# Optimization experiments

Hardware: AMD Instinct MI355X
Metric: run time of the kernel (lower is better)

The kernel has to match this reference:

```python
import math
import jax, jax.numpy as jnp
import numpy as np

B, L, DM = 2, 1024, 1024
STATE, EXPAND, CONV, DTR = 16, 2, 4, 8
INNER = DM * EXPAND          # 2048
NFFT = L // 2 + 1            # 513


def _silu(v):
    return v * jax.nn.sigmoid(v)


def setup_inputs() -> dict:
    key = jax.random.key(0)
    ks = jax.random.split(key, 12)
    s = lambda k, shape, sc=0.02: (jax.random.normal(k, shape, jnp.float32) * sc)
    # dt_proj bias initialized like the torch module: exp(U(0,1)*(log dt_max - log dt_min) + log dt_min)
    inv_dt = jnp.exp(jax.random.uniform(ks[10], (INNER,), jnp.float32)
                     * (math.log(0.1) - math.log(0.001)) + math.log(0.001))
    return {
        "x": jax.random.normal(ks[0], (B, L, DM), jnp.float32),
        "in_proj_w": s(ks[1], (2 * INNER, DM)),
        "conv_w": s(ks[2], (INNER, 1, CONV), 0.1),      # depthwise conv kernel
        "conv_b": jnp.zeros((INNER,), jnp.float32),
        "A_log": jnp.tile(jnp.log(jnp.arange(1, STATE + 1, dtype=jnp.float32)), (INNER, 1)),
        "D": jnp.ones((INNER,), jnp.float32),
        "x_proj_w": s(ks[3], (DTR + 2 * STATE, INNER)),
        "dt_proj_w": s(ks[4], (INNER, DTR)),
        "dt_proj_b": inv_dt,
        "filter_real": s(ks[5], (INNER, NFFT)),
        "filter_imag": s(ks[6], (INNER, NFFT)),
        "spectral_decay": jnp.ones((INNER,), jnp.float32) * 0.01,
        "fusion_w": s(ks[7], (INNER, 2 * INNER)),
        "fusion_b": jnp.zeros((INNER,), jnp.float32),
        "out_proj_w": s(ks[8], (DM, INNER)),
        "ln_gamma": jnp.ones((DM,), jnp.float32),
        "ln_beta": jnp.zeros((DM,), jnp.float32),
    }


def reference(x, in_proj_w, conv_w, conv_b, A_log, D, x_proj_w, dt_proj_w, dt_proj_b,
              filter_real, filter_imag, spectral_decay, fusion_w, fusion_b,
              out_proj_w, ln_gamma, ln_beta):
    residual = x
    xz = x @ in_proj_w.T                                   # [B,L,2*INNER]
    x_inner, z = xz[..., :INNER], xz[..., INNER:]
    z = _silu(z)

    # ---- SSM path ----
    xc = jnp.swapaxes(x_inner, 1, 2)                       # [B,E,L]
    xc = jax.lax.conv_general_dilated(
        xc, conv_w, (1,), [(CONV - 1, 0)],                 # causal depthwise conv (pad-left == torch pad + truncate)
        dimension_numbers=("NCH", "OIH", "NCH"),
        feature_group_count=INNER) + conv_b[None, :, None]
    x_conv = jnp.swapaxes(_silu(xc), 1, 2)                 # [B,L,E]

    x_dbc = x_conv @ x_proj_w.T                            # [B,L,DTR+2S]
    dt_x = x_dbc[..., :DTR]
    Bm = x_dbc[..., DTR:DTR + STATE]                       # [B,L,S]
    Cm = x_dbc[..., DTR + STATE:]                          # [B,L,S]
    dt = jax.nn.softplus(dt_x @ dt_proj_w.T + dt_proj_b)   # [B,L,E]
    A = -jnp.exp(A_log)                                    # [E,S]
    dA = jnp.exp(dt[..., None] * A)                        # [B,L,E,S]
    dBx = (dt * x_conv)[..., None] * Bm[:, :, None, :]     # [B,L,E,S]

    def step(h, inp):
        dA_t, dBx_t, C_t = inp
        h = dA_t * h + dBx_t                               # [B,E,S]
        return h, jnp.einsum('bes,bs->be', h, C_t)

    h0 = jnp.zeros((B, INNER, STATE), x.dtype)
    _, ys = jax.lax.scan(step, h0,
                         (jnp.swapaxes(dA, 0, 1), jnp.swapaxes(dBx, 0, 1), jnp.swapaxes(Cm, 0, 1)))
    y_ssm = jnp.swapaxes(ys, 0, 1) + x_conv * D            # [B,L,E]

    # ---- Spectral path ----
    xf = jnp.fft.rfft(jnp.swapaxes(x_inner, 1, 2), axis=-1)        # [B,E,NFFT]
    freqs = jnp.linspace(0.0, 1.0, NFFT)
    filt = (filter_real + 1j * filter_imag) * jnp.exp(-spectral_decay[:, None] * freqs[None, :])
    y_spec = jnp.swapaxes(jnp.fft.irfft(xf * filt[None], n=L, axis=-1), 1, 2)  # [B,L,E]

    # ---- Gated fusion ----
    g = jax.nn.sigmoid(jnp.concatenate([y_ssm, y_spec], -1) @ fusion_w.T + fusion_b)
    y = g * y_ssm + (1.0 - g) * y_spec
    y = y * z
    out = y @ out_proj_w.T + residual                      # [B,L,DM]

    mu = out.mean(-1, keepdims=True)
    var = out.var(-1, keepdims=True)
    return (out - mu) / jnp.sqrt(var + 1e-5) * ln_gamma + ln_beta
```

## Files before the change

### kernel.cpp

```cpp
#include <hip/hip_runtime.h>
#include <math.h>

#define B_ 2
#define L_ 1024
#define DM_ 1024
#define STATE_ 16
#define CONV_ 4
#define DTR_ 8
#define INNER_ 2048
#define M_ (B_*L_)
#define MD_ (B_*INNER_)
#define NFFT_ 513
#define NFP_ 1152
#define NCH_ 32
#define CHL_ 32
#define SK_ 32
#define KSL_ (2048/SK_)

typedef unsigned short u16;
typedef __attribute__((ext_vector_type(8))) short short8;
typedef __attribute__((ext_vector_type(8))) __bf16 bf16x8;
typedef __attribute__((ext_vector_type(4))) float f32x4;

__device__ __forceinline__ float frcp_(float x) { return __builtin_amdgcn_rcpf(x); }
__device__ __forceinline__ float fexp_(float x) { return __expf(x); }
__device__ __forceinline__ float fsigm_(float x) { return frcp_(1.f + __expf(-x)); }
__device__ __forceinline__ float fsilu_(float x) { return x * frcp_(1.f + __expf(-x)); }
__device__ __forceinline__ float fsoftplus_(float v) {
  return (v > 20.f) ? v : __logf(1.f + __expf(v));
}
__device__ __forceinline__ u16 f2bf(float f) {
  union { float f; unsigned u; } v; v.f = f;
  unsigned r = v.u + 0x7fffu + ((v.u >> 16) & 1u);
  return (u16)(r >> 16);
}
__device__ __forceinline__ float bf2f(u16 h) {
  union { unsigned u; float f; } v; v.u = ((unsigned)h) << 16;
  return v.f;
}
__device__ __forceinline__ void gload16(const void* g, void* l) {
  __builtin_amdgcn_global_load_lds(
      (const __attribute__((address_space(1))) unsigned*)g,
      (__attribute__((address_space(3))) unsigned*)l, 16, 0, 0);
}
__device__ __forceinline__ f32x4 mfma_bf16(short8 a, short8 b, f32x4 c) {
  return __builtin_amdgcn_mfma_f32_16x16x32_bf16(
      __builtin_bit_cast(bf16x8, a), __builtin_bit_cast(bf16x8, b), c, 0, 0, 0);
}

#define CVT_N0 2097152
#define CVT_N1 6291456
#define CVT_N2 14680064
#define CVT_NT 16777216
__global__ __launch_bounds__(256) void cvt4_k(
    const float* __restrict__ s0, const float* __restrict__ s1,
    const float* __restrict__ s2, const float* __restrict__ s3,
    u16* __restrict__ out)
{
  int i = (blockIdx.x*256 + threadIdx.x) * 4;
  const float* src; int off;
  if (i < CVT_N0)      { src = s0; off = 0; }
  else if (i < CVT_N1) { src = s1; off = CVT_N0; }
  else if (i < CVT_N2) { src = s2; off = CVT_N1; }
  else                 { src = s3; off = CVT_N2; }
  float4 v = *(const float4*)(src + (i - off));
  ushort4 o;
  o.x = f2bf(v.x); o.y = f2bf(v.y); o.z = f2bf(v.z); o.w = f2bf(v.w);
  *(ushort4*)(out + i) = o;
}

template<int TM, int TN, int EPI>
__global__ __launch_bounds__((TM/64)*(TN/32)*64) void mgemm_k(
    const u16* __restrict__ Ab, const u16* __restrict__ Bb,
    void* __restrict__ Cout, int K, int ldc,
    const float* __restrict__ aux0, const u16* __restrict__ aux1,
    const float* __restrict__ aux2, const float* __restrict__ aux3)
{
  constexpr int WN   = TN/32;
  constexpr int NW   = (TM/64)*WN;
  constexpr int NTHR = NW*64;
  __shared__ __align__(16) u16 As[2][TM*64];
  __shared__ __align__(16) u16 Bs[2][TN*64];
  const int t = threadIdx.x;
  const int lane = t & 63;
  const int w = t >> 6;
  const int wm = w / WN, wn = w % WN;
  const int M0 = blockIdx.y * TM, N0 = blockIdx.x * TN;

  f32x4 acc[4][2] = {};

  auto stage = [&](int buf, int k0) {
    #pragma unroll
    for (int q = 0; q < TM*8/NTHR; q++) {
      int u = q*NTHR + t;
      int row = u >> 3, gpr = u & 7;
      int grp = gpr ^ (row & 7);
      gload16(Ab + (size_t)(M0+row)*K + k0 + grp*8, &As[buf][u*8]);
    }
    #pragma unroll
    for (int q = 0; q < TN*8/NTHR; q++) {
      int u = q*NTHR + t;
      int row = u >> 3, gpr = u & 7;
      int grp = gpr ^ (row & 7);
      gload16(Bb + (size_t)(N0+row)*K + k0 + grp*8, &Bs[buf][u*8]);
    }
  };

  stage(0, 0);
  const int nk = K >> 6;
  for (int ks = 0; ks < nk; ks++) {
    const int buf = ks & 1;
    __syncthreads();
    if (ks + 1 < nk) stage(buf ^ 1, (ks + 1) << 6);
    const u16* Asb = As[buf];
    const u16* Bsb = Bs[buf];
    #pragma unroll
    for (int kk = 0; kk < 2; kk++) {
      const int quad = lane >> 4;
      const int grp = kk*4 + quad;
      short8 af[4], bf[2];
      #pragma unroll
      for (int i = 0; i < 4; i++) {
        int row = wm*64 + i*16 + (lane & 15);
        af[i] = *(const short8*)&Asb[(row*8 + (grp ^ (row & 7)))*8];
      }
      #pragma unroll
      for (int j = 0; j < 2; j++) {
        int row = wn*32 + j*16 + (lane & 15);
        bf[j] = *(const short8*)&Bsb[(row*8 + (grp ^ (row & 7)))*8];
      }
      #pragma unroll
      for (int i = 0; i < 4; i++)
        #pragma unroll
        for (int j = 0; j < 2; j++)
          acc[i][j] = mfma_bf16(af[i], bf[j], acc[i][j]);
    }
  }

  #pragma unroll
  for (int i = 0; i < 4; i++) {
    int mbase = M0 + wm*64 + i*16 + (lane >> 4)*4;
    #pragma unroll
    for (int j = 0; j < 2; j++) {
      int n = N0 + wn*32 + j*16 + (lane & 15);
      #pragma unroll
      for (int r = 0; r < 4; r++) {
        int m = mbase + r;
        float v = acc[i][j][r];
        if (EPI == 0) {
          ((float*)Cout)[(size_t)m*ldc + n] = v;
        } else if (EPI == 1) {
          float g  = fsigm_(v + aux0[n]);
          float ys = bf2f(aux1[(size_t)m*4096 + n]);
          float yp = bf2f(aux1[(size_t)m*4096 + 2048 + n]);
          float z  = aux2[(size_t)m*4096 + 2048 + n];
          ((u16*)Cout)[(size_t)m*ldc + n] = f2bf((g*ys + (1.f-g)*yp)*fsilu_(z));
        } else if (EPI == 2) {
          ((float*)Cout)[(size_t)m*ldc + n] = v + aux2[(size_t)m*ldc + n];
        } else if (EPI == 3) {
          float pv = __shfl_xor(v, 1, 64);
          int f = n >> 1;
          float outv = 0.f;
          if (f < NFFT_) {
            int c = m & (INNER_-1);
            float d  = fexp_(-aux2[c] * (float)f * (1.f/512.f));
            float wr = aux0[c*NFFT_+f]*d, wi = aux3[c*NFFT_+f]*d;
            float a = (n & 1) ? pv : v;
            float b = (n & 1) ? v : pv;
            outv = (n & 1) ? (a*wi + b*wr) : (a*wr - b*wi);
          }
          ((u16*)Cout)[(size_t)m*ldc + n] = f2bf(outv);
        } else {
          ((u16*)Cout)[(size_t)m*ldc + n] = f2bf(v);
        }
      }
    }
  }
}

__global__ __launch_bounds__(256) void xproj_k(
    const float* __restrict__ xconv, const float* __restrict__ W,
    float* __restrict__ part)
{
  __shared__ float Bs[40][KSL_+4];
  const int sk = blockIdx.x, mt = blockIdx.y;
  const int k0 = sk*KSL_;
  for (int i = threadIdx.x; i < 40*KSL_; i += 256) {
    int n = i >> 6, k = i & (KSL_-1);
    Bs[n][k] = W[(size_t)n*2048 + k0 + k];
  }
  __syncthreads();
  const int m = mt*256 + threadIdx.x;
  const float* arow = xconv + (size_t)m*2048 + k0;
  float acc[40];
  #pragma unroll
  for (int j=0;j<40;j++) acc[j]=0.f;
  for (int k = 0; k < KSL_; k += 4) {
    float4 a = *(const float4*)(arow + k);
    #pragma unroll
    for (int j = 0; j < 40; j++) {
      float4 b = *(const float4*)&Bs[j][k];
      acc[j] += a.x*b.x + a.y*b.y + a.z*b.z + a.w*b.w;
    }
  }
  float* o = part + ((size_t)sk*M_ + m)*40;
  #pragma unroll
  for (int j = 0; j < 10; j++)
    *(float4*)(o + j*4) = make_float4(acc[j*4], acc[j*4+1], acc[j*4+2], acc[j*4+3]);
}

__global__ __launch_bounds__(256) void xpred_k(const float* __restrict__ part,
                                               float* __restrict__ xdbc)
{
  int i = blockIdx.x*256 + threadIdx.x;
  float s = 0.f;
  #pragma unroll
  for (int sk = 0; sk < SK_; sk++) s += part[(size_t)sk*81920 + i];
  xdbc[i] = s;
}

__global__ __launch_bounds__(256) void conv_silu_k(
    const float* __restrict__ xz, const float* __restrict__ cw,
    const float* __restrict__ cb, float* __restrict__ xc)
{
  int idx = blockIdx.x*256 + threadIdx.x;
  int c = idx & (INNER_-1);
  int m = idx >> 11;
  int l = m & (L_-1);
  const float* base = xz + (size_t)m*4096 + c;
  float w0=cw[c*4+0], w1=cw[c*4+1], w2=cw[c*4+2], w3=cw[c*4+3];
  float s = cb[c] + w3*base[0];
  if (l >= 1) s += w2*base[-4096];
  if (l >= 2) s += w1*base[-2*4096];
  if (l >= 3) s += w0*base[-3*4096];
  xc[(size_t)m*INNER_ + c] = fsilu_(s);
}

__global__ __launch_bounds__(256) void scan1_k(
    const float* __restrict__ xdbc, const float* __restrict__ xconv,
    const float* __restrict__ A_log, const float* __restrict__ dtw,
    const float* __restrict__ dtb, float* __restrict__ Pq)
{
  int idx = blockIdx.x*256 + threadIdx.x;
  int e  = idx & (INNER_-1);
  int bc = idx >> 11;
  int ch = bc & (NCH_-1);
  int b  = bc >> 5;
  float A[STATE_];
  #pragma unroll
  for (int s=0;s<STATE_;s++) A[s] = -fexp_(A_log[e*STATE_+s]);
  float w[DTR_];
  #pragma unroll
  for (int r=0;r<DTR_;r++) w[r] = dtw[e*DTR_+r];
  float bias = dtb[e];
  float h[STATE_] = {};
  float sdt = 0.f;
  int mbase = b*L_ + ch*CHL_;
  for (int l=0;l<CHL_;l++) {
    int m = mbase + l;
    const float* row = xdbc + (size_t)m*40;
    float v = bias;
    #pragma unroll
    for (int r=0;r<DTR_;r++) v += row[r]*w[r];
    float dt = fsoftplus_(v);
    sdt += dt;
    float dx = dt * xconv[(size_t)m*INNER_ + e];
    #pragma unroll
    for (int s=0;s<STATE_;s++) {
      float dA = fexp_(dt*A[s]);
      h[s] = dA*h[s] + dx*row[8+s];
    }
  }
  float* o = Pq + (size_t)idx*32;
  #pragma unroll
  for (int s=0;s<STATE_;s++) { o[s] = fexp_(A[s]*sdt); o[16+s] = h[s]; }
}

__global__ __launch_bounds__(256) void scan2_k(float* __restrict__ Pq)
{
  int idx = blockIdx.x*256 + threadIdx.x;
  int s = idx & 15;
  int e = (idx >> 4) & (INNER_-1);
  int b = idx >> 15;
  float h = 0.f;
  for (int ch = 0; ch < NCH_; ch++) {
    size_t base = ((size_t)(b*NCH_+ch)*INNER_ + e)*32;
    float p = Pq[base + s];
    float q = Pq[base + 16 + s];
    Pq[base + 16 + s] = h;
    h = p*h + q;
  }
}

__global__ __launch_bounds__(256) void scan3_k(
    const float* __restrict__ xdbc, const float* __restrict__ xconv,
    const float* __restrict__ A_log, const float* __restrict__ dtw,
    const float* __restrict__ dtb, const float* __restrict__ Dp,
    const float* __restrict__ Pq, u16* __restrict__ ycat)
{
  int idx = blockIdx.x*256 + threadIdx.x;
  int e  = idx & (INNER_-1);
  int bc = idx >> 11;
  int ch = bc & (NCH_-1);
  int b  = bc >> 5;
  float A[STATE_];
  #pragma unroll
  for (int s=0;s<STATE_;s++) A[s] = -fexp_(A_log[e*STATE_+s]);
  float w[DTR_];
  #pragma unroll
  for (int r=0;r<DTR_;r++) w[r] = dtw[e*DTR_+r];
  float bias = dtb[e];
  float Dv = Dp[e];
  float h[STATE_];
  const float* hi = Pq + (size_t)idx*32 + 16;
  #pragma unroll
  for (int s=0;s<STATE_;s++) h[s] = hi[s];
  int mbase = b*L_ + ch*CHL_;
  for (int l=0;l<CHL_;l++) {
    int m = mbase + l;
    const float* row = xdbc + (size_t)m*40;
    float v = bias;
    #pragma unroll
    for (int r=0;r<DTR_;r++) v += row[r]*w[r];
    float dt = fsoftplus_(v);
    float xcv = xconv[(size_t)m*INNER_ + e];
    float dx = dt * xcv;
    float y = 0.f;
    #pragma unroll
    for (int s=0;s<STATE_;s++) {
      float dA = fexp_(dt*A[s]);
      h[s] = dA*h[s] + dx*row[8+s];
      y += h[s]*row[24+s];
    }
    ycat[(size_t)m*4096 + e] = f2bf(y + xcv*Dv);
  }
}

__global__ __launch_bounds__(256) void transpose_fwd_k(const float* __restrict__ xz,
                                                       u16* __restrict__ xt)
{
  __shared__ float tile[32][33];
  int tx = threadIdx.x & 31, ty = threadIdx.x >> 5;
  int l0 = blockIdx.x*32, c0 = blockIdx.y*32, b = blockIdx.z;
  #pragma unroll
  for (int j=0;j<4;j++) {
    int l = l0 + ty + j*8;
    tile[ty+j*8][tx] = xz[(size_t)(b*L_+l)*4096 + (c0+tx)];
  }
  __syncthreads();
  #pragma unroll
  for (int j=0;j<4;j++) {
    int c = c0 + ty + j*8;
    xt[(size_t)(b*INNER_+c)*L_ + (l0+tx)] = f2bf(tile[tx][ty+j*8]);
  }
}

__global__ __launch_bounds__(256) void transpose_bwd_k(const u16* __restrict__ yt,
                                                       u16* __restrict__ ycat)
{
  __shared__ float tile[32][33];
  int tx = threadIdx.x & 31, ty = threadIdx.x >> 5;
  int l0 = blockIdx.x*32, c0 = blockIdx.y*32, b = blockIdx.z;
  #pragma unroll
  for (int j=0;j<4;j++) {
    int c = c0 + ty + j*8;
    tile[ty+j*8][tx] = bf2f(yt[(size_t)(b*INNER_+c)*L_ + (l0+tx)]);
  }
  __syncthreads();
  #pragma unroll
  for (int j=0;j<4;j++) {
    int l = l0 + ty + j*8;
    ycat[(size_t)(b*L_+l)*4096 + 2048 + (c0+tx)] = f2bf(tile[tx][ty+j*8]);
  }
}

__global__ __launch_bounds__(256) void genWdftb_k(u16* __restrict__ W) {
  int idx = blockIdx.x*256 + threadIdx.x;
  int l = idx & (L_-1);
  int col = idx >> 10;
  float v = 0.f;
  int f = col >> 1;
  if (f < NFFT_) {
    int ph = (l*f) & (L_-1);
    float th = (float)ph * (6.283185307179586f / (float)L_);
    v = (col & 1) ? -__sinf(th) : __cosf(th);
  }
  W[idx] = f2bf(v);
}

__global__ __launch_bounds__(256) void genWinvb_k(u16* __restrict__ W) {
  int idx = blockIdx.x*256 + threadIdx.x;
  int r = idx % NFP_;
  int l = idx / NFP_;
  int f = r >> 1;
  float v = 0.f;
  if (f < NFFT_) {
    bool edge = (f == 0) || (f == 512);
    float sc = (edge ? 1.f : 2.f) / (float)L_;
    int ph = (f*l) & (L_-1);
    float th = (float)ph * (6.283185307179586f / (float)L_);
    if (r & 1) v = edge ? 0.f : -sc*__sinf(th);
    else       v = sc*__cosf(th);
  }
  W[idx] = f2bf(v);
}

__global__ __launch_bounds__(256) void ln_k(const float* __restrict__ inp,
    const float* __restrict__ gma, const float* __restrict__ bta,
    float* __restrict__ out)
{
  int m = blockIdx.x;
  const float* row = inp + (size_t)m*DM_;
  float s=0.f, s2=0.f;
  float v[4];
  #pragma unroll
  for (int j=0;j<4;j++) {
    v[j] = row[threadIdx.x + j*256];
    s += v[j]; s2 += v[j]*v[j];
  }
  #pragma unroll
  for (int off=32; off>=1; off>>=1) {
    s  += __shfl_down(s, off);
    s2 += __shfl_down(s2, off);
  }
  __shared__ float rs[4], rs2[4], stats[2];
  int wid = threadIdx.x >> 6;
  if ((threadIdx.x & 63) == 0) { rs[wid]=s; rs2[wid]=s2; }
  __syncthreads();
  if (threadIdx.x == 0) {
    float ts  = rs[0]+rs[1]+rs[2]+rs[3];
    float ts2 = rs2[0]+rs2[1]+rs2[2]+rs2[3];
    float mu  = ts/(float)DM_;
    float var = ts2/(float)DM_ - mu*mu;
    stats[0] = mu; stats[1] = rsqrtf(var + 1e-5f);
  }
  __syncthreads();
  float mu = stats[0], rstd = stats[1];
  #pragma unroll
  for (int j=0;j<4;j++) {
    int n = threadIdx.x + j*256;
    out[(size_t)m*DM_ + n] = (v[j]-mu)*rstd*gma[n] + bta[n];
  }
}

extern "C" void kernel_launch(void* const* d_in, const int* in_sizes, int n_in,
                              void* d_out, int out_size, void* d_ws, size_t ws_size,
                              hipStream_t stream)
{
  const float* x       = (const float*)d_in[0];
  const float* in_w    = (const float*)d_in[1];
  const float* conv_w  = (const float*)d_in[2];
  const float* conv_b  = (const float*)d_in[3];
  const float* A_log   = (const float*)d_in[4];
  const float* Dp      = (const float*)d_in[5];
  const float* xproj_w = (const float*)d_in[6];
  const float* dt_w    = (const float*)d_in[7];
  const float* dt_b    = (const float*)d_in[8];
  const float* f_re    = (const float*)d_in[9];
  const float* f_im    = (const float*)d_in[10];
  const float* s_dec   = (const float*)d_in[11];
  const float* fus_w   = (const float*)d_in[12];
  const float* fus_b   = (const float*)d_in[13];
  const float* out_w   = (const float*)d_in[14];
  const float* ln_g    = (const float*)d_in[15];
  const float* ln_b    = (const float*)d_in[16];
  float* out = (float*)d_out;

  float* ws    = (float*)d_ws;
  float* xz    = ws;
  float* xconv = xz    + 8388608;
  float* xdbc  = xconv + 4194304;
  float* Pq    = xdbc  + 81920;
  u16* ub      = (u16*)(Pq + 4194304);
  u16* xb      = ub;
  u16* inwb    = xb    + 2097152;
  u16* fuswb   = inwb  + 4194304;
  u16* outwb   = fuswb + 8388608;
  u16* xt      = outwb + 2097152;
  u16* Wb      = xt    + 4194304;
  u16* XFb     = Wb    + 1179648;
  u16* ycat    = XFb   + 4718592;
  u16* yt      = inwb;
  u16* ycomb   = xt;
  float* outp  = xconv;
  float* part  = (float*)ycat;

  cvt4_k<<<CVT_NT/1024, 256, 0, stream>>>(x, in_w, fus_w, out_w, xb);

  mgemm_k<128,128,0><<<dim3(4096/128, M_/128), 512, 0, stream>>>(
      xb, inwb, xz, 1024, 4096, nullptr, nullptr, nullptr, nullptr);
  conv_silu_k<<<(M_*INNER_)/256, 256, 0, stream>>>(xz, conv_w, conv_b, xconv);
  xproj_k<<<dim3(SK_, M_/256), 256, 0, stream>>>(xconv, xproj_w, part);
  xpred_k<<<(M_*40)/256, 256, 0, stream>>>(part, xdbc);
  scan1_k<<<(B_*NCH_*INNER_)/256, 256, 0, stream>>>(xdbc, xconv, A_log, dt_w, dt_b, Pq);
  scan2_k<<<(B_*INNER_*STATE_)/256, 256, 0, stream>>>(Pq);
  scan3_k<<<(B_*NCH_*INNER_)/256, 256, 0, stream>>>(xdbc, xconv, A_log, dt_w, dt_b, Dp, Pq, ycat);
  transpose_fwd_k<<<dim3(L_/32, INNER_/32, B_), 256, 0, stream>>>(xz, xt);
  genWdftb_k<<<(NFP_*1024)/256, 256, 0, stream>>>(Wb);
  mgemm_k<128,64,3><<<dim3(NFP_/64, MD_/128), 256, 0, stream>>>(
      xt, Wb, XFb, 1024, NFP_, f_re, nullptr, s_dec, f_im);
  genWinvb_k<<<(NFP_*1024)/256, 256, 0, stream>>>(Wb);
  mgemm_k<128,64,4><<<dim3(1024/64, MD_/128), 256, 0, stream>>>(
      XFb, Wb, yt, NFP_, 1024, nullptr, nullptr, nullptr, nullptr);
  transpose_bwd_k<<<dim3(L_/32, INNER_/32, B_), 256, 0, stream>>>(yt, ycat);
  mgemm_k<128,64,1><<<dim3(2048/64, M_/128), 256, 0, stream>>>(
      ycat, fuswb, ycomb, 4096, 2048, fus_b, ycat, xz, nullptr);
  mgemm_k<64,64,2><<<dim3(1024/64, M_/64), 128, 0, stream>>>(
      ycomb, outwb, outp, 2048, 1024, nullptr, nullptr, x, nullptr);
  ln_k<<<M_, 256, 0, stream>>>(outp, ln_g, ln_b, out);
}
```

Baseline: 443.2 us.

## Fuse transposes into GEMM epilogues, register-block conv, prefetch scan rows

The in-projection GEMM epilogue now also writes a transposed bf16 copy of x_inner for the DFT GEMM, and the inverse-DFT GEMM epilogue writes directly into the transposed ycat slot. This removes both standalone transpose kernels and their extra global round trips. The depthwise conv now computes 8 timesteps per thread from 11 loaded values, cutting redundant loads. The scan kernels prefetch the next row's dt/B/C and xconv into registers. The trade-off is that the transposed epilogue stores are strided and uncoalesced, and register pressure rises in the scan kernels.

```diff
diff --git a/kernel.cpp b/kernel.cpp
--- a/kernel.cpp
+++ b/kernel.cpp
@@ -73,7 +73,7 @@
 __global__ __launch_bounds__((TM/64)*(TN/32)*64) void mgemm_k(
     const u16* __restrict__ Ab, const u16* __restrict__ Bb,
     void* __restrict__ Cout, int K, int ldc,
-    const float* __restrict__ aux0, const u16* __restrict__ aux1,
+    const float* __restrict__ aux0, u16* __restrict__ aux1,
     const float* __restrict__ aux2, const float* __restrict__ aux3)
 {
   constexpr int WN   = TN/32;
@@ -170,8 +170,15 @@
             outv = (n & 1) ? (a*wi + b*wr) : (a*wr - b*wi);
           }
           ((u16*)Cout)[(size_t)m*ldc + n] = f2bf(outv);
+        } else if (EPI == 5) {
+          ((float*)Cout)[(size_t)m*ldc + n] = v;
+          if (n < 2048) {
+            int b2 = m >> 10, l2 = m & 1023;
+            aux1[((size_t)(b2*2048 + n) << 10) + l2] = f2bf(v);
+          }
         } else {
-          ((u16*)Cout)[(size_t)m*ldc + n] = f2bf(v);
+          int b2 = m >> 11, c2 = m & (INNER_-1);
+          ((u16*)Cout)[((size_t)((b2 << 10) + n) << 12) + 2048 + c2] = f2bf(v);
         }
       }
     }
@@ -225,15 +232,22 @@
 {
   int idx = blockIdx.x*256 + threadIdx.x;
   int c = idx & (INNER_-1);
-  int m = idx >> 11;
-  int l = m & (L_-1);
-  const float* base = xz + (size_t)m*4096 + c;
+  int g = idx >> 11;
+  int b = g >> 7;
+  int lb = (g & 127) * 8;
   float w0=cw[c*4+0], w1=cw[c*4+1], w2=cw[c*4+2], w3=cw[c*4+3];
-  float s = cb[c] + w3*base[0];
-  if (l >= 1) s += w2*base[-4096];
-  if (l >= 2) s += w1*base[-2*4096];
-  if (l >= 3) s += w0*base[-3*4096];
-  xc[(size_t)m*INNER_ + c] = fsilu_(s);
+  float bias = cb[c];
+  float v[11];
+  #pragma unroll
+  for (int j = 0; j < 11; j++) {
+    int l = lb - 3 + j;
+    v[j] = (l >= 0) ? xz[((size_t)((b << 10) + l))*4096 + c] : 0.f;
+  }
+  #pragma unroll
+  for (int j = 0; j < 8; j++) {
+    float s = bias + w0*v[j] + w1*v[j+1] + w2*v[j+2] + w3*v[j+3];
+    xc[((size_t)((b << 10) + lb + j))*INNER_ + c] = fsilu_(s);
+  }
 }
 
 __global__ __launch_bounds__(256) void scan1_k(
@@ -256,20 +270,46 @@
   float h[STATE_] = {};
   float sdt = 0.f;
   int mbase = b*L_ + ch*CHL_;
+  float dtx[DTR_], Bv[STATE_], xcv;
+  {
+    const float* row = xdbc + (size_t)mbase*40;
+    #pragma unroll
+    for (int r=0;r<DTR_;r++) dtx[r] = row[r];
+    #pragma unroll
+    for (int s=0;s<STATE_;s++) Bv[s] = row[8+s];
+    xcv = xconv[(size_t)mbase*INNER_ + e];
+  }
   for (int l=0;l<CHL_;l++) {
-    int m = mbase + l;
-    const float* row = xdbc + (size_t)m*40;
+    float ndtx[DTR_], nBv[STATE_], nxcv = 0.f;
+    if (l+1 < CHL_) {
+      const float* nrow = xdbc + (size_t)(mbase+l+1)*40;
+      #pragma unroll
+      for (int r=0;r<DTR_;r++) ndtx[r] = nrow[r];
+      #pragma unroll
+      for (int s=0;s<STATE_;s++) nBv[s] = nrow[8+s];
+      nxcv = xconv[(size_t)(mbase+l+1)*INNER_ + e];
+    } else {
+      #pragma unroll
+      for (int r=0;r<DTR_;r++) ndtx[r] = 0.f;
+      #pragma unroll
+      for (int s=0;s<STATE_;s++) nBv[s] = 0.f;
+    }
     float v = bias;
     #pragma unroll
-    for (int r=0;r<DTR_;r++) v += row[r]*w[r];
+    for (int r=0;r<DTR_;r++) v += dtx[r]*w[r];
     float dt = fsoftplus_(v);
     sdt += dt;
-    float dx = dt * xconv[(size_t)m*INNER_ + e];
+    float dx = dt * xcv;
     #pragma unroll
     for (int s=0;s<STATE_;s++) {
       float dA = fexp_(dt*A[s]);
-      h[s] = dA*h[s] + dx*row[8+s];
-    }
+      h[s] = dA*h[s] + dx*Bv[s];
+    }
+    #pragma unroll
+    for (int r=0;r<DTR_;r++) dtx[r] = ndtx[r];
+    #pragma unroll
+    for (int s=0;s<STATE_;s++) Bv[s] = nBv[s];
+    xcv = nxcv;
   }
   float* o = Pq + (size_t)idx*32;
   #pragma unroll
@@ -316,61 +356,48 @@
   #pragma unroll
   for (int s=0;s<STATE_;s++) h[s] = hi[s];
   int mbase = b*L_ + ch*CHL_;
+  float dtx[DTR_], Bv[STATE_], Cv[STATE_], xcv;
+  {
+    const float* row = xdbc + (size_t)mbase*40;
+    #pragma unroll
+    for (int r=0;r<DTR_;r++) dtx[r] = row[r];
+    #pragma unroll
+    for (int s=0;s<STATE_;s++) { Bv[s] = row[8+s]; Cv[s] = row[24+s]; }
+    xcv = xconv[(size_t)mbase*INNER_ + e];
+  }
   for (int l=0;l<CHL_;l++) {
-    int m = mbase + l;
-    const float* row = xdbc + (size_t)m*40;
+    float ndtx[DTR_], nBv[STATE_], nCv[STATE_], nxcv = 0.f;
+    if (l+1 < CHL_) {
+      const float* nrow = xdbc + (size_t)(mbase+l+1)*40;
+      #pragma unroll
+      for (int r=0;r<DTR_;r++) ndtx[r] = nrow[r];
+      #pragma unroll
+      for (int s=0;s<STATE_;s++) { nBv[s] = nrow[8+s]; nCv[s] = nrow[24+s]; }
+      nxcv = xconv[(size_t)(mbase+l+1)*INNER_ + e];
+    } else {
+      #pragma unroll
+      for (int r=0;r<DTR_;r++) ndtx[r] = 0.f;
+      #pragma unroll
+      for (int s=0;s<STATE_;s++) { nBv[s] = 0.f; nCv[s] = 0.f; }
+    }
     float v = bias;
     #pragma unroll
-    for (int r=0;r<DTR_;r++) v += row[r]*w[r];
+    for (int r=0;r<DTR_;r++) v += dtx[r]*w[r];
     float dt = fsoftplus_(v);
-    float xcv = xconv[(size_t)m*INNER_ + e];
     float dx = dt * xcv;
     float y = 0.f;
     #pragma unroll
     for (int s=0;s<STATE_;s++) {
       float dA = fexp_(dt*A[s]);
-      h[s] = dA*h[s] + dx*row[8+s];
-      y += h[s]*row[24+s];
-    }
-    ycat[(size_t)m*4096 + e] = f2bf(y + xcv*Dv);
-  }
-}
-
-__global__ __launch_bounds__(256) void transpose_fwd_k(const float* __restrict__ xz,
-                                                       u16* __restrict__ xt)
-{
-  __shared__ float tile[32][33];
-  int tx = threadIdx.x & 31, ty = threadIdx.x >> 5;
-  int l0 = blockIdx.x*32, c0 = blockIdx.y*32, b = blockIdx.z;
-  #pragma unroll
-  for (int j=0;j<4;j++) {
-    int l = l0 + ty + j*8;
-    tile[ty+j*8][tx] = xz[(size_t)(b*L_+l)*4096 + (c0+tx)];
-  }
-  __syncthreads();
-  #pragma unroll
-  for (int j=0;j<4;j++) {
-    int c = c0 + ty + j*8;
-    xt[(size_t)(b*INNER_+c)*L_ + (l0+tx)] = f2bf(tile[tx][ty+j*8]);
-  }
-}
-
-__global__ __launch_bounds__(256) void transpose_bwd_k(const u16* __restrict__ yt,
-                                                       u16* __restrict__ ycat)
-{
-  __shared__ float tile[32][33];
-  int tx = threadIdx.x & 31, ty = threadIdx.x >> 5;
-  int l0 = blockIdx.x*32, c0 = blockIdx.y*32, b = blockIdx.z;
-  #pragma unroll
-  for (int j=0;j<4;j++) {
-    int c = c0 + ty + j*8;
-    tile[ty+j*8][tx] = bf2f(yt[(size_t)(b*INNER_+c)*L_ + (l0+tx)]);
-  }
-  __syncthreads();
-  #pragma unroll
-  for (int j=0;j<4;j++) {
-    int l = l0 + ty + j*8;
-    ycat[(size_t)(b*L_+l)*4096 + 2048 + (c0+tx)] = f2bf(tile[tx][ty+j*8]);
+      h[s] = dA*h[s] + dx*Bv[s];
+      y += h[s]*Cv[s];
+    }
+    ycat[(size_t)(mbase+l)*4096 + e] = f2bf(y + xcv*Dv);
+    #pragma unroll
+    for (int r=0;r<DTR_;r++) dtx[r] = ndtx[r];
+    #pragma unroll
+    for (int s=0;s<STATE_;s++) { Bv[s] = nBv[s]; Cv[s] = nCv[s]; }
+    xcv = nxcv;
   }
 }
 
@@ -480,29 +507,26 @@
   u16* Wb      = xt    + 4194304;
   u16* XFb     = Wb    + 1179648;
   u16* ycat    = XFb   + 4718592;
-  u16* yt      = inwb;
   u16* ycomb   = xt;
   float* outp  = xconv;
   float* part  = (float*)ycat;
 
   cvt4_k<<<CVT_NT/1024, 256, 0, stream>>>(x, in_w, fus_w, out_w, xb);
 
-  mgemm_k<128,128,0><<<dim3(4096/128, M_/128), 512, 0, stream>>>(
-      xb, inwb, xz, 1024, 4096, nullptr, nullptr, nullptr, nullptr);
-  conv_silu_k<<<(M_*INNER_)/256, 256, 0, stream>>>(xz, conv_w, conv_b, xconv);
+  mgemm_k<128,128,5><<<dim3(4096/128, M_/128), 512, 0, stream>>>(
+      xb, inwb, xz, 1024, 4096, nullptr, xt, nullptr, nullptr);
+  conv_silu_k<<<(M_*INNER_/8)/256, 256, 0, stream>>>(xz, conv_w, conv_b, xconv);
   xproj_k<<<dim3(SK_, M_/256), 256, 0, stream>>>(xconv, xproj_w, part);
   xpred_k<<<(M_*40)/256, 256, 0, stream>>>(part, xdbc);
   scan1_k<<<(B_*NCH_*INNER_)/256, 256, 0, stream>>>(xdbc, xconv, A_log, dt_w, dt_b, Pq);
   scan2_k<<<(B_*INNER_*STATE_)/256, 256, 0, stream>>>(Pq);
   scan3_k<<<(B_*NCH_*INNER_)/256, 256, 0, stream>>>(xdbc, xconv, A_log, dt_w, dt_b, Dp, Pq, ycat);
-  transpose_fwd_k<<<dim3(L_/32, INNER_/32, B_), 256, 0, stream>>>(xz, xt);
   genWdftb_k<<<(NFP_*1024)/256, 256, 0, stream>>>(Wb);
   mgemm_k<128,64,3><<<dim3(NFP_/64, MD_/128), 256, 0, stream>>>(
       xt, Wb, XFb, 1024, NFP_, f_re, nullptr, s_dec, f_im);
   genWinvb_k<<<(NFP_*1024)/256, 256, 0, stream>>>(Wb);
-  mgemm_k<128,64,4><<<dim3(1024/64, MD_/128), 256, 0, stream>>>(
-      XFb, Wb, yt, NFP_, 1024, nullptr, nullptr, nullptr, nullptr);
-  transpose_bwd_k<<<dim3(L_/32, INNER_/32, B_), 256, 0, stream>>>(yt, ycat);
+  mgemm_k<128,64,6><<<dim3(1024/64, MD_/128), 256, 0, stream>>>(
+      XFb, Wb, ycat, NFP_, 0, nullptr, nullptr, nullptr, nullptr);
   mgemm_k<128,64,1><<<dim3(2048/64, M_/128), 256, 0, stream>>>(
       ycat, fuswb, ycomb, 4096, 2048, fus_b, ycat, xz, nullptr);
   mgemm_k<64,64,2><<<dim3(1024/64, M_/64), 128, 0, stream>>>(
```

Result: faster. 410.5 us (-7.4%).
